# Performance work log

Hardware: AMD Instinct MI355X
Metric: run time of the kernel (lower is better)

## Reference

```python
import jax, jax.numpy as jnp
import numpy as np


def _split_box(v):
    # BoxTensor.from_vector: split last dim into (min z, max Z)
    D = v.shape[-1] // 2
    return v[..., :D], v[..., D:]


def setup_inputs() -> dict:
    key = jax.random.key(0)
    k1, k2 = jax.random.split(key)
    men_embeds = jax.random.normal(k1, (256, 128), dtype=jnp.float32)
    all_en_embeds = jax.random.normal(k2, (20000, 128), dtype=jnp.float32)
    return {"men_embeds": men_embeds, "all_en_embeds": all_en_embeds}


def reference(men_embeds, all_en_embeds):
    # men boxes: [M, D] min/max ; entity boxes: [N, D] min/max
    zm, Zm = _split_box(men_embeds)
    ze, Ze = _split_box(all_en_embeds)
    # intersection box per (mention, candidate): [M, N, D]
    lo = jnp.maximum(zm[:, None, :], ze[None, :, :])
    hi = jnp.minimum(Zm[:, None, :], Ze[None, :, :])
    # soft volume: prod_d softplus(side) -> log-volume = sum log softplus
    log_int_vol = jnp.sum(jnp.log(jax.nn.softplus(hi - lo)), axis=-1)   # [M, N]
    log_men_vol = jnp.sum(jnp.log(jax.nn.softplus(Zm - zm)), axis=-1)   # [M]
    # containment log prob = log vol(men ∩ en) - log vol(men); logits = exp(.)
    return jnp.exp(log_int_vol - log_men_vol[:, None])
```

## Files before the change

kernel.cpp:

```cpp
#include <hip/hip_runtime.h>


#define BM 32
#define BN 128
#define DD 64

#define FD(PIJ, EMc, IMc, EEc, IEc) PIJ *= __log2f(1.0f + fminf(EMc, EEc) * fminf(IMc, IEc));

__global__ __launch_bounds__(512, 4)
void ivr_kernel(const float* __restrict__ men, const float* __restrict__ en,
                float* __restrict__ out, int M, int N) {
    __shared__ __align__(16) float2 sMen[DD][BM];
    __shared__ __align__(16) float  sEe[DD][BN];
    __shared__ __align__(16) float  sIe[DD][BN];

    const int tx = threadIdx.x;
    const int m0 = blockIdx.y * BM;
    const int n0 = blockIdx.x * BN;

    float rden;
    {
        const int ml = tx >> 4;
        const int dc = (tx & 15) * 4;
        int mm = m0 + ml; if (mm >= M) mm = M - 1;
        const float* r = men + (size_t)mm * 128 + dc;
        const float4 z = *reinterpret_cast<const float4*>(r);
        const float4 Z = *reinterpret_cast<const float4*>(r + 64);
        float Em, Im, prod;
        Em = __expf(Z.x); Im = __expf(-z.x); sMen[dc + 0][ml] = make_float2(Em, Im); prod  = __log2f(1.0f + Em * Im);
        Em = __expf(Z.y); Im = __expf(-z.y); sMen[dc + 1][ml] = make_float2(Em, Im); prod *= __log2f(1.0f + Em * Im);
        Em = __expf(Z.z); Im = __expf(-z.z); sMen[dc + 2][ml] = make_float2(Em, Im); prod *= __log2f(1.0f + Em * Im);
        Em = __expf(Z.w); Im = __expf(-z.w); sMen[dc + 3][ml] = make_float2(Em, Im); prod *= __log2f(1.0f + Em * Im);
        prod *= __shfl_xor(prod, 1);
        prod *= __shfl_xor(prod, 2);
        prod *= __shfl_xor(prod, 4);
        prod *= __shfl_xor(prod, 8);
        rden = 1.0f / prod;
    }
    {
        const int nl = tx >> 2;
        const int c4 = tx & 3;
        int nn = n0 + nl; if (nn >= N) nn = N - 1;
        const float* r = en + (size_t)nn * 128 + c4 * 16;
#define ESTG4(I) { \
        const float4 z_ = *reinterpret_cast<const float4*>(r + (I) * 4); \
        const float4 Z_ = *reinterpret_cast<const float4*>(r + 64 + (I) * 4); \
        const int d_ = c4 * 16 + (I) * 4; \
        sEe[d_ + 0][nl] = __expf(Z_.x); sIe[d_ + 0][nl] = __expf(-z_.x); \
        sEe[d_ + 1][nl] = __expf(Z_.y); sIe[d_ + 1][nl] = __expf(-z_.y); \
        sEe[d_ + 2][nl] = __expf(Z_.z); sIe[d_ + 2][nl] = __expf(-z_.z); \
        sEe[d_ + 3][nl] = __expf(Z_.w); sIe[d_ + 3][nl] = __expf(-z_.w); }
        ESTG4(0) ESTG4(1) ESTG4(2) ESTG4(3)
#undef ESTG4
    }
    __syncthreads();

    const int ni = (tx & 31) * 4;
    const int mi = (tx >> 5) * 2;

    const float oden = __shfl_xor(rden, 16);
    const int hib = (tx >> 4) & 1;
    const float rd0 = hib ? oden : rden;
    const float rd1 = hib ? rden : oden;

    float p[2][4];
    #pragma unroll
    for (int i = 0; i < 2; ++i)
        #pragma unroll
        for (int j = 0; j < 4; ++j) p[i][j] = 1.0f;

    #pragma unroll 1
    for (int c = 0; c < 8; ++c) {
        #pragma unroll
        for (int k = 0; k < 8; ++k) {
            const int d = c * 8 + k;
            const float4 mf  = *reinterpret_cast<const float4*>(&sMen[d][mi]);
            const float4 Ee4 = *reinterpret_cast<const float4*>(&sEe[d][ni]);
            const float4 Ie4 = *reinterpret_cast<const float4*>(&sIe[d][ni]);
            FD(p[0][0], mf.x, mf.y, Ee4.x, Ie4.x)
            FD(p[0][1], mf.x, mf.y, Ee4.y, Ie4.y)
            FD(p[0][2], mf.x, mf.y, Ee4.z, Ie4.z)
            FD(p[0][3], mf.x, mf.y, Ee4.w, Ie4.w)
            FD(p[1][0], mf.z, mf.w, Ee4.x, Ie4.x)
            FD(p[1][1], mf.z, mf.w, Ee4.y, Ie4.y)
            FD(p[1][2], mf.z, mf.w, Ee4.z, Ie4.z)
            FD(p[1][3], mf.z, mf.w, Ee4.w, Ie4.w)
        }
    }

    #pragma unroll
    for (int j = 0; j < 4; ++j) { p[0][j] *= rd0; p[1][j] *= rd1; }

    #pragma unroll
    for (int i = 0; i < 2; ++i) {
        const int m = m0 + mi + i;
        if (m >= M) continue;
        const int n = n0 + ni;
        if (n + 4 <= N) {
            *reinterpret_cast<float4*>(&out[(size_t)m * N + n]) =
                make_float4(p[i][0], p[i][1], p[i][2], p[i][3]);
        } else {
            #pragma unroll
            for (int j = 0; j < 4; ++j)
                if (n + j < N) out[(size_t)m * N + n + j] = p[i][j];
        }
    }
}

extern "C" void kernel_launch(void* const* d_in, const int* in_sizes, int n_in,
                              void* d_out, int out_size, void* d_ws, size_t ws_size,
                              hipStream_t stream) {
    const float* men = (const float*)d_in[0];
    const float* en  = (const float*)d_in[1];
    float* out = (float*)d_out;
    const int M = in_sizes[0] / 128;
    const int N = in_sizes[1] / 128;
    dim3 grid((N + BN - 1) / BN, (M + BM - 1) / BM);
    ivr_kernel<<<grid, dim3(512), 0, stream>>>(men, en, out, M, N);
}
```

Measured before the change: 136.0 us.

## Switch block tile to 64x64 and use fma inside log2 argument

Changes the block tile from 32 mentions x 128 entities to 64x64. This halves the number of entity rows each block loads and exponentiates, at the cost of twice as many mention rows per block. The staging loops and the thread mapping for both inputs are rewritten to match, including the shuffle pattern that reduces the per-mention denominator. The 1+a*b inside the log2 is also folded into a single fma. The square tile changes the redundant exp work and LDS access patterns, and the compute per block stays the same.

```diff
diff --git a/kernel.cpp b/kernel.cpp
--- a/kernel.cpp
+++ b/kernel.cpp
@@ -1,11 +1,12 @@
 #include <hip/hip_runtime.h>
 
 
-#define BM 32
-#define BN 128
+#define BM 64
+#define BN 64
 #define DD 64
 
-#define FD(PIJ, EMc, IMc, EEc, IEc) PIJ *= __log2f(1.0f + fminf(EMc, EEc) * fminf(IMc, IEc));
+#define FD(PIJ, EMc, IMc, EEc, IEc) \
+    PIJ *= __log2f(__builtin_fmaf(fminf(EMc, EEc), fminf(IMc, IEc), 1.0f));
 
 __global__ __launch_bounds__(512, 4)
 void ivr_kernel(const float* __restrict__ men, const float* __restrict__ en,
@@ -20,46 +21,51 @@
 
     float rden;
     {
-        const int ml = tx >> 4;
-        const int dc = (tx & 15) * 4;
+        const int ml  = tx >> 3;
+        const int dcM = (tx & 7) * 8;
         int mm = m0 + ml; if (mm >= M) mm = M - 1;
-        const float* r = men + (size_t)mm * 128 + dc;
-        const float4 z = *reinterpret_cast<const float4*>(r);
-        const float4 Z = *reinterpret_cast<const float4*>(r + 64);
+        const float* r = men + (size_t)mm * 128 + dcM;
+        const float4 z0 = *reinterpret_cast<const float4*>(r);
+        const float4 z1 = *reinterpret_cast<const float4*>(r + 4);
+        const float4 Z0 = *reinterpret_cast<const float4*>(r + 64);
+        const float4 Z1 = *reinterpret_cast<const float4*>(r + 68);
         float Em, Im, prod;
-        Em = __expf(Z.x); Im = __expf(-z.x); sMen[dc + 0][ml] = make_float2(Em, Im); prod  = __log2f(1.0f + Em * Im);
-        Em = __expf(Z.y); Im = __expf(-z.y); sMen[dc + 1][ml] = make_float2(Em, Im); prod *= __log2f(1.0f + Em * Im);
-        Em = __expf(Z.z); Im = __expf(-z.z); sMen[dc + 2][ml] = make_float2(Em, Im); prod *= __log2f(1.0f + Em * Im);
-        Em = __expf(Z.w); Im = __expf(-z.w); sMen[dc + 3][ml] = make_float2(Em, Im); prod *= __log2f(1.0f + Em * Im);
+#define MSTG(K, ZV, ZZ) { Em = __expf(ZZ); Im = __expf(-(ZV)); \
+        sMen[dcM + (K)][ml] = make_float2(Em, Im); \
+        prod *= __log2f(__builtin_fmaf(Em, Im, 1.0f)); }
+        Em = __expf(Z0.x); Im = __expf(-z0.x);
+        sMen[dcM + 0][ml] = make_float2(Em, Im);
+        prod = __log2f(__builtin_fmaf(Em, Im, 1.0f));
+        MSTG(1, z0.y, Z0.y) MSTG(2, z0.z, Z0.z) MSTG(3, z0.w, Z0.w)
+        MSTG(4, z1.x, Z1.x) MSTG(5, z1.y, Z1.y) MSTG(6, z1.z, Z1.z) MSTG(7, z1.w, Z1.w)
+#undef MSTG
         prod *= __shfl_xor(prod, 1);
         prod *= __shfl_xor(prod, 2);
         prod *= __shfl_xor(prod, 4);
-        prod *= __shfl_xor(prod, 8);
         rden = 1.0f / prod;
     }
     {
-        const int nl = tx >> 2;
-        const int c4 = tx & 3;
+        const int nl  = tx & 63;
+        const int dcE = (tx >> 6) * 8;
         int nn = n0 + nl; if (nn >= N) nn = N - 1;
-        const float* r = en + (size_t)nn * 128 + c4 * 16;
-#define ESTG4(I) { \
-        const float4 z_ = *reinterpret_cast<const float4*>(r + (I) * 4); \
-        const float4 Z_ = *reinterpret_cast<const float4*>(r + 64 + (I) * 4); \
-        const int d_ = c4 * 16 + (I) * 4; \
-        sEe[d_ + 0][nl] = __expf(Z_.x); sIe[d_ + 0][nl] = __expf(-z_.x); \
-        sEe[d_ + 1][nl] = __expf(Z_.y); sIe[d_ + 1][nl] = __expf(-z_.y); \
-        sEe[d_ + 2][nl] = __expf(Z_.z); sIe[d_ + 2][nl] = __expf(-z_.z); \
-        sEe[d_ + 3][nl] = __expf(Z_.w); sIe[d_ + 3][nl] = __expf(-z_.w); }
-        ESTG4(0) ESTG4(1) ESTG4(2) ESTG4(3)
-#undef ESTG4
+        const float* r = en + (size_t)nn * 128 + dcE;
+        const float4 z0 = *reinterpret_cast<const float4*>(r);
+        const float4 z1 = *reinterpret_cast<const float4*>(r + 4);
+        const float4 Z0 = *reinterpret_cast<const float4*>(r + 64);
+        const float4 Z1 = *reinterpret_cast<const float4*>(r + 68);
+#define ESTG(K, ZV, ZZ) { sEe[dcE + (K)][nl] = __expf(ZZ); \
+                          sIe[dcE + (K)][nl] = __expf(-(ZV)); }
+        ESTG(0, z0.x, Z0.x) ESTG(1, z0.y, Z0.y) ESTG(2, z0.z, Z0.z) ESTG(3, z0.w, Z0.w)
+        ESTG(4, z1.x, Z1.x) ESTG(5, z1.y, Z1.y) ESTG(6, z1.z, Z1.z) ESTG(7, z1.w, Z1.w)
+#undef ESTG
     }
     __syncthreads();
 
-    const int ni = (tx & 31) * 4;
-    const int mi = (tx >> 5) * 2;
+    const int ni = (tx & 15) * 4;
+    const int mi = (tx >> 4) * 2;
 
-    const float oden = __shfl_xor(rden, 16);
-    const int hib = (tx >> 4) & 1;
+    const float oden = __shfl_xor(rden, 8);
+    const int hib = (tx >> 3) & 1;
     const float rd0 = hib ? oden : rden;
     const float rd1 = hib ? rden : oden;
 
```

After: 133.1 us. -2.1%, faster.
